# Optimization experiments

Hardware: AMD Instinct MI355X
Metric: run time of the kernel (lower is better)

## Reference

```python
import jax, jax.numpy as jnp
import numpy as np

EMBED = 3072
NQ = 32
NKV = 8
HD = EMBED // NQ  # 96
GROUPS = NQ // NKV  # 4
ROPE_BASE = 10000.0


def apply_rope(t, positions):
    # t: [b, h, s, d]; positions: [s] int
    d = t.shape[-1]
    inv_freq = 1.0 / (ROPE_BASE ** (jnp.arange(0, d, 2, dtype=jnp.float32) / d))  # [d/2]
    ang = positions.astype(jnp.float32)[:, None] * inv_freq[None, :]  # [s, d/2]
    cos = jnp.cos(ang)[None, None]  # [1,1,s,d/2]
    sin = jnp.sin(ang)[None, None]
    t1, t2 = t[..., : d // 2], t[..., d // 2 :]
    return jnp.concatenate([t1 * cos - t2 * sin, t2 * cos + t1 * sin], axis=-1)


def setup_inputs() -> dict:
    key = jax.random.key(0)
    k1, k2, k3 = jax.random.split(key, 3)
    b, s = 2, 2048
    x = jax.random.normal(k1, (b, s, EMBED), dtype=jnp.float32)
    positions = jnp.arange(s, dtype=jnp.int32)
    mask = jnp.triu(jnp.ones((s, s), dtype=bool), k=1)  # True = masked (causal)
    qkv_size = NQ * HD + 2 * NKV * HD  # 4608
    W_qkv = jax.random.normal(k2, (qkv_size, EMBED), dtype=jnp.float32) * (EMBED ** -0.5)
    W_o = jax.random.normal(k3, (EMBED, EMBED), dtype=jnp.float32) * (EMBED ** -0.5)
    return {"x": x, "positions": positions, "mask": mask, "W_qkv": W_qkv, "W_o": W_o}


def reference(x, positions, mask, W_qkv, W_o):
    b, s, _ = x.shape
    scaling = HD ** -0.5
    qkv = x @ W_qkv.T  # [b, s, 4608]
    q_size, kv_size = NQ * HD, NKV * HD
    q = qkv[..., :q_size].reshape(b, s, NQ, HD).transpose(0, 2, 1, 3)          # [b,NQ,s,d]
    k = qkv[..., q_size : q_size + kv_size].reshape(b, s, NKV, HD).transpose(0, 2, 1, 3)
    v = qkv[..., q_size + kv_size :].reshape(b, s, NKV, HD).transpose(0, 2, 1, 3)
    q = apply_rope(q, positions)
    k = apply_rope(k, positions)
    q = q.reshape(b, NKV, GROUPS, s, HD)
    scores = jnp.einsum("bkgsd,bktd->bkgst", q, k) * scaling  # [b,NKV,G,s,s]
    scores = jnp.where(mask[None, None, None], -jnp.inf, scores)
    attn = jax.nn.softmax(scores, axis=-1)
    out = jnp.einsum("bkgst,bktd->bkgsd", attn, v)
    out = out.reshape(b, NQ, s, HD).transpose(0, 2, 1, 3).reshape(b, s, NQ * HD)
    return out @ W_o.T
```

## Files before the change

kernel.cpp:

```cpp
#include <hip/hip_runtime.h>
#include <cstdint>

typedef unsigned short u16;
typedef unsigned int u32;
typedef __attribute__((ext_vector_type(4))) float f32x4;
typedef __attribute__((ext_vector_type(8))) __bf16 bf16x8;
typedef __attribute__((ext_vector_type(8))) unsigned short u16x8;
typedef __attribute__((ext_vector_type(4))) unsigned int u32x4;

#define S_LEN 2048
#define BATCH 2
#define NQH 32
#define NKVH 8
#define HD 96
#define EMB 3072
#define QKVN 4608
#define KOFF 3072
#define VOFF 3840
#define KSP 104

__device__ __forceinline__ u16 f2b(float f) {
    u32 u = __float_as_uint(f);
    u32 r = (u + 0x7fffu + ((u >> 16) & 1u)) >> 16;
    return (u16)r;
}
__device__ __forceinline__ float b2f(u16 h) { return __uint_as_float(((u32)h) << 16); }
__device__ __forceinline__ u32 cvtpk(float lo, float hi) {
    u32 r;
    asm("v_cvt_pk_bf16_f32 %0, %1, %2" : "=v"(r) : "v"(lo), "v"(hi));
    return r;
}

__global__ __launch_bounds__(256) void conv_f2b(const float* __restrict__ in,
                                                u16* __restrict__ outp, int n8) {
    const int i = blockIdx.x * 256 + threadIdx.x;
    if (i >= n8) return;
    const f32x4* q = (const f32x4*)(in + (size_t)i * 8);
    const f32x4 a = q[0], b = q[1];
    u16x8 t;
#pragma unroll
    for (int j = 0; j < 4; ++j) {
        t[j] = f2b(a[j]);
        t[j + 4] = f2b(b[j]);
    }
    *(u16x8*)(outp + (size_t)i * 8) = t;
}

typedef __attribute__((address_space(1))) const uint32_t gas_u32;
typedef __attribute__((address_space(3))) uint32_t las_u32;
__device__ __forceinline__ void gld_lds16(const u16* g, u16* l) {
    __builtin_amdgcn_global_load_lds((gas_u32*)g, (las_u32*)l, 16, 0, 0);
}

#define WAITV4 asm volatile("s_waitcnt vmcnt(4)" ::: "memory")
#define WAITV0 asm volatile("s_waitcnt vmcnt(0)" ::: "memory")
#define BARRIER __builtin_amdgcn_s_barrier()
#define SCHEDB __builtin_amdgcn_sched_barrier(0)

template <bool OUTF32>
__global__ __launch_bounds__(256, 2) void gemm_bt_p(const u16* __restrict__ Ap,
                                                    const u16* __restrict__ Bp,
                                                    void* __restrict__ Cp,
                                                    int M, int N, int K, int ldc) {
    __shared__ __align__(16) u16 S[2 * 16384];
    const int tid = threadIdx.x;
    const int wave = tid >> 6, lane = tid & 63;
    const int lrow = lane & 15, lhi = lane >> 4;

    int bxi = blockIdx.x, byi = blockIdx.y;
    {
        const int gx = gridDim.x;
        const int nwg = gx * gridDim.y;
        if ((nwg & 7) == 0) {
            int fid = byi * gx + bxi;
            fid = (fid & 7) * (nwg >> 3) + (fid >> 3);
            bxi = fid % gx;
            byi = fid / gx;
        }
    }
    const int bm = byi * 128, bn = bxi * 128;
    const int wm = (wave >> 1) * 64, wn = (wave & 1) * 64;
    const int xsl = ((lhi ^ (lrow & 3) ^ ((lrow >> 2) & 3)) << 3);
    const int srow = tid >> 2;
    const int scol = (((tid & 3) ^ ((tid >> 2) & 3) ^ ((tid >> 4) & 3))) * 8;
    const u16* gA0 = Ap + (size_t)(bm + srow) * K + scol;
    const u16* gA1 = Ap + (size_t)(bm + 64 + srow) * K + scol;
    const u16* gB0 = Bp + (size_t)(bn + srow) * K + scol;
    const u16* gB1 = Bp + (size_t)(bn + 64 + srow) * K + scol;
    u16* const dbase = S + (tid & 192) * 8;

    f32x4 acc[4][4] = {};
    const int nt = K >> 6;

    gld_lds16(gA0, dbase);
    gld_lds16(gA1, dbase + 2048);
    gld_lds16(gB0, dbase + 8192);
    gld_lds16(gB1, dbase + 8192 + 2048);
    gld_lds16(gA0 + 32, dbase + 4096);
    gld_lds16(gA1 + 32, dbase + 4096 + 2048);
    gld_lds16(gB0 + 32, dbase + 8192 + 4096);
    gld_lds16(gB1 + 32, dbase + 8192 + 4096 + 2048);

    for (int t = 0; t + 1 < nt; ++t) {
        const int cur = t & 1;
        const u16* Ab = S + cur * 16384;
        const u16* Bb = Ab + 8192;
        u16* dn = dbase + (cur ^ 1) * 16384;
        const int ko = (t + 1) << 6;

        WAITV4;
        BARRIER;
        SCHEDB;
        gld_lds16(gA0 + ko, dn);
        gld_lds16(gA1 + ko, dn + 2048);
        bf16x8 af[4], bf0[2], bf1[2];
#pragma unroll
        for (int mi = 0; mi < 4; ++mi)
            af[mi] = *(const bf16x8*)(Ab + (wm + mi * 16 + lrow) * 32 + xsl);
#pragma unroll
        for (int ni = 0; ni < 2; ++ni)
            bf0[ni] = *(const bf16x8*)(Bb + (wn + ni * 16 + lrow) * 32 + xsl);
        __builtin_amdgcn_s_setprio(1);
#pragma unroll
        for (int mi = 0; mi < 4; ++mi)
#pragma unroll
            for (int ni = 0; ni < 2; ++ni)
                acc[mi][ni] = __builtin_amdgcn_mfma_f32_16x16x32_bf16(af[mi], bf0[ni],
                                                                      acc[mi][ni], 0, 0, 0);
        __builtin_amdgcn_s_setprio(0);
        gld_lds16(gB0 + ko, dn + 8192);
        gld_lds16(gB1 + ko, dn + 8192 + 2048);
#pragma unroll
        for (int ni = 0; ni < 2; ++ni)
            bf1[ni] = *(const bf16x8*)(Bb + (wn + (ni + 2) * 16 + lrow) * 32 + xsl);
        __builtin_amdgcn_s_setprio(1);
#pragma unroll
        for (int mi = 0; mi < 4; ++mi)
#pragma unroll
            for (int ni = 0; ni < 2; ++ni)
                acc[mi][ni + 2] = __builtin_amdgcn_mfma_f32_16x16x32_bf16(af[mi], bf1[ni],
                                                                          acc[mi][ni + 2], 0, 0, 0);
        __builtin_amdgcn_s_setprio(0);

        WAITV4;
        BARRIER;
        SCHEDB;
        gld_lds16(gA0 + ko + 32, dn + 4096);
        gld_lds16(gA1 + ko + 32, dn + 4096 + 2048);
#pragma unroll
        for (int mi = 0; mi < 4; ++mi)
            af[mi] = *(const bf16x8*)(Ab + 4096 + (wm + mi * 16 + lrow) * 32 + xsl);
#pragma unroll
        for (int ni = 0; ni < 2; ++ni)
            bf0[ni] = *(const bf16x8*)(Bb + 4096 + (wn + ni * 16 + lrow) * 32 + xsl);
        __builtin_amdgcn_s_setprio(1);
#pragma unroll
        for (int mi = 0; mi < 4; ++mi)
#pragma unroll
            for (int ni = 0; ni < 2; ++ni)
                acc[mi][ni] = __builtin_amdgcn_mfma_f32_16x16x32_bf16(af[mi], bf0[ni],
                                                                      acc[mi][ni], 0, 0, 0);
        __builtin_amdgcn_s_setprio(0);
        gld_lds16(gB0 + ko + 32, dn + 8192 + 4096);
        gld_lds16(gB1 + ko + 32, dn + 8192 + 4096 + 2048);
#pragma unroll
        for (int ni = 0; ni < 2; ++ni)
            bf1[ni] = *(const bf16x8*)(Bb + 4096 + (wn + (ni + 2) * 16 + lrow) * 32 + xsl);
        __builtin_amdgcn_s_setprio(1);
#pragma unroll
        for (int mi = 0; mi < 4; ++mi)
#pragma unroll
            for (int ni = 0; ni < 2; ++ni)
                acc[mi][ni + 2] = __builtin_amdgcn_mfma_f32_16x16x32_bf16(af[mi], bf1[ni],
                                                                          acc[mi][ni + 2], 0, 0, 0);
        __builtin_amdgcn_s_setprio(0);
    }

    {
        const int cur = (nt - 1) & 1;
        const u16* Ab = S + cur * 16384;
        const u16* Bb = Ab + 8192;
        WAITV4;
        BARRIER;
        SCHEDB;
        bf16x8 af[4], bfr[4];
#pragma unroll
        for (int mi = 0; mi < 4; ++mi)
            af[mi] = *(const bf16x8*)(Ab + (wm + mi * 16 + lrow) * 32 + xsl);
#pragma unroll
        for (int ni = 0; ni < 4; ++ni)
            bfr[ni] = *(const bf16x8*)(Bb + (wn + ni * 16 + lrow) * 32 + xsl);
#pragma unroll
        for (int mi = 0; mi < 4; ++mi)
#pragma unroll
            for (int ni = 0; ni < 4; ++ni)
                acc[mi][ni] = __builtin_amdgcn_mfma_f32_16x16x32_bf16(af[mi], bfr[ni],
                                                                      acc[mi][ni], 0, 0, 0);
        WAITV0;
        BARRIER;
        SCHEDB;
#pragma unroll
        for (int mi = 0; mi < 4; ++mi)
            af[mi] = *(const bf16x8*)(Ab + 4096 + (wm + mi * 16 + lrow) * 32 + xsl);
#pragma unroll
        for (int ni = 0; ni < 4; ++ni)
            bfr[ni] = *(const bf16x8*)(Bb + 4096 + (wn + ni * 16 + lrow) * 32 + xsl);
#pragma unroll
        for (int mi = 0; mi < 4; ++mi)
#pragma unroll
            for (int ni = 0; ni < 4; ++ni)
                acc[mi][ni] = __builtin_amdgcn_mfma_f32_16x16x32_bf16(af[mi], bfr[ni],
                                                                      acc[mi][ni], 0, 0, 0);
    }

    const int orow = bm + wm + lhi * 4;
    const int ocol = bn + wn + lrow;
#pragma unroll
    for (int mi = 0; mi < 4; ++mi)
#pragma unroll
        for (int ni = 0; ni < 4; ++ni)
#pragma unroll
            for (int r = 0; r < 4; ++r) {
                const size_t idx = (size_t)(orow + mi * 16 + r) * ldc + ocol + ni * 16;
                if constexpr (OUTF32)
                    ((float*)Cp)[idx] = acc[mi][ni][r];
                else
                    ((u16*)Cp)[idx] = f2b(acc[mi][ni][r]);
            }
}

__global__ __launch_bounds__(256) void gqa_rope(u16* __restrict__ qkv,
                                                const int* __restrict__ positions) {
    int i = blockIdx.x * 256 + threadIdx.x;
    const int pair = i % 48;
    int t = i / 48;
    const int head = t % (NQH + NKVH);
    const int bs = t / (NQH + NKVH);
    const int pos = positions[bs & (S_LEN - 1)];
    const size_t base = (size_t)bs * QKVN + (head < NQH ? head * HD : KOFF + (head - NQH) * HD);
    const float invf = __expf(-(float)(2 * pair) * (1.0f / 96.0f) * 9.210340371976184f);
    const float ang = (float)pos * invf;
    float sn, cs;
    __sincosf(ang, &sn, &cs);
    const float t1 = b2f(qkv[base + pair]);
    const float t2 = b2f(qkv[base + 48 + pair]);
    qkv[base + pair] = f2b(t1 * cs - t2 * sn);
    qkv[base + 48 + pair] = f2b(t2 * cs + t1 * sn);
}

__global__ __launch_bounds__(256) void gqa_attn5(const u16* __restrict__ qkv,
                                                 u16* __restrict__ out) {
    __shared__ __align__(16) u16 Ks[64 * KSP];
    __shared__ __align__(16) u16 Vtmp[64 * 96];
    __shared__ __align__(16) u16 Vt[96 * 72];

    const int tid = threadIdx.x;
    const int wave = tid >> 6, lane = tid & 63;
    const int lrow = lane & 15, lhi = lane >> 4;
    const int bx = blockIdx.x;
    const int qt32 = 63 - (bx >> 4);
    const int kvh = (bx >> 1) & 7, bb = bx & 1;
    const int qh = kvh * 4 + wave;
    const int srow0 = bb * S_LEN + qt32 * 32;
    const int kb_last = (qt32 * 32 + 31) >> 6;
    const float cl2 = 0.10206207261596575f * 1.4426950408889634f;

    bf16x8 bq[2][3];
#pragma unroll
    for (int qt = 0; qt < 2; ++qt)
#pragma unroll
        for (int kd = 0; kd < 3; ++kd)
            bq[qt][kd] = *(const bf16x8*)(qkv + (size_t)(srow0 + qt * 16 + lrow) * QKVN +
                                          qh * 96 + kd * 32 + lhi * 8);

    float m_s[2] = {-3e38f, -3e38f}, l_s[2] = {0.0f, 0.0f};
    f32x4 oacc[6][2] = {};

    const int s0 = lrow + ((lane & 16) ? 32 : 0);
    const int s1 = s0 + 16;
    const bool khi = (lane & 32) != 0;

    const size_t kvrow0 = (size_t)(bb * S_LEN) * QKVN;
    u16x8 kreg[3], vreg[3];

    {
        const size_t kbase = kvrow0 + KOFF + (size_t)kvh * 96;
        const size_t vbase = kvrow0 + VOFF + (size_t)kvh * 96;
#pragma unroll
        for (int i = 0; i < 3; ++i) {
            const int u = tid + 256 * i;
            const int so = (u % 12) * 8, sr = u / 12;
            kreg[i] = *(const u16x8*)(qkv + kbase + (size_t)sr * QKVN + so);
            vreg[i] = *(const u16x8*)(qkv + vbase + (size_t)sr * QKVN + so);
        }
#pragma unroll
        for (int i = 0; i < 3; ++i) {
            const int u = tid + 256 * i;
            const int so = (u % 12) * 8, sr = u / 12;
            *(u16x8*)(Ks + sr * KSP + so) = kreg[i];
            *(u16x8*)(Vtmp + sr * 96 + so) = vreg[i];
        }
        __syncthreads();
#pragma unroll
        for (int i = 0; i < 3; ++i) {
            const int u = tid + 256 * i;
            const int td = u % 96, ts8 = u / 96;
            u16x8 c;
#pragma unroll
            for (int j = 0; j < 8; ++j) c[j] = Vtmp[(ts8 * 8 + j) * 96 + td];
            *(u16x8*)(Vt + td * 72 + ts8 * 8) = c;
        }
    }

    for (int kb = 0; kb <= kb_last; ++kb) {
        if (kb < kb_last) {
            const size_t kbase2 = kvrow0 + (size_t)((kb + 1) * 64) * QKVN + KOFF + kvh * 96;
            const size_t vbase2 = kvrow0 + (size_t)((kb + 1) * 64) * QKVN + VOFF + kvh * 96;
#pragma unroll
            for (int i = 0; i < 3; ++i) {
                const int u = tid + 256 * i;
                const int so = (u % 12) * 8, sr = u / 12;
                kreg[i] = *(const u16x8*)(qkv + kbase2 + (size_t)sr * QKVN + so);
                vreg[i] = *(const u16x8*)(qkv + vbase2 + (size_t)sr * QKVN + so);
            }
        }
        __syncthreads();

        bf16x8 ka[4][3];
#pragma unroll
        for (int kt = 0; kt < 4; ++kt)
#pragma unroll
            for (int kd = 0; kd < 3; ++kd)
                ka[kt][kd] = *(const bf16x8*)(Ks + (kt * 16 + lrow) * KSP + kd * 32 + lhi * 8);

        const int qoff = qt32 * 32 - kb * 64;
        const bool lastkb = (kb == kb_last);
        u32 bp[2][2][4];

#pragma unroll
        for (int qt = 0; qt < 2; ++qt) {
            const int qrelmax = qoff + qt * 16 + 15;
            f32x4 sacc[4] = {};
#pragma unroll
            for (int kt = 0; kt < 4; ++kt) {
                if (lastkb && kt * 16 > qrelmax) continue;
#pragma unroll
                for (int kd = 0; kd < 3; ++kd)
                    sacc[kt] = __builtin_amdgcn_mfma_f32_16x16x32_bf16(ka[kt][kd], bq[qt][kd],
                                                                       sacc[kt], 0, 0, 0);
            }
            float p[4][4];
            float mx = -3e38f;
            if (lastkb) {
                const int qrel = qoff + qt * 16 + lrow;
#pragma unroll
                for (int kt = 0; kt < 4; ++kt)
#pragma unroll
                    for (int r = 0; r < 4; ++r) {
                        const bool live = (kt * 16 + lhi * 4 + r) <= qrel;
                        const float s = live ? sacc[kt][r] : -3e38f;
                        p[kt][r] = s;
                        mx = fmaxf(mx, s);
                    }
            } else {
#pragma unroll
                for (int kt = 0; kt < 4; ++kt)
#pragma unroll
                    for (int r = 0; r < 4; ++r) {
                        p[kt][r] = sacc[kt][r];
                        mx = fmaxf(mx, sacc[kt][r]);
                    }
            }
            mx = fmaxf(mx, __shfl_xor(mx, 16));
            mx = fmaxf(mx, __shfl_xor(mx, 32));
            float mn = m_s[qt];
            if (!__all(mx - mn <= 20.0f)) {
                const float mnew = fmaxf(mn, mx);
                const float alpha = exp2f((mn - mnew) * cl2);
                m_s[qt] = mnew;
                mn = mnew;
                l_s[qt] *= alpha;
#pragma unroll
                for (int dt = 0; dt < 6; ++dt)
#pragma unroll
                    for (int r = 0; r < 4; ++r) oacc[dt][qt][r] *= alpha;
            }
            float rs = 0.0f;
#pragma unroll
            for (int kt = 0; kt < 4; ++kt)
#pragma unroll
                for (int r = 0; r < 4; ++r) {
                    const float pv = exp2f((p[kt][r] - mn) * cl2);
                    p[kt][r] = pv;
                    rs += pv;
                }
            rs += __shfl_xor(rs, 16);
            rs += __shfl_xor(rs, 32);
            l_s[qt] += rs;
            u32 pk[4][2];
#pragma unroll
            for (int kt = 0; kt < 4; ++kt) {
                pk[kt][0] = cvtpk(p[kt][0], p[kt][1]);
                pk[kt][1] = cvtpk(p[kt][2], p[kt][3]);
            }
#pragma unroll
            for (int kk = 0; kk < 2; ++kk) {
                const u32 a0 = (u32)__shfl((int)pk[kk * 2][0], s0, 64);
                const u32 b0 = (u32)__shfl((int)pk[kk * 2 + 1][0], s0, 64);
                const u32 a1 = (u32)__shfl((int)pk[kk * 2][1], s0, 64);
                const u32 b1 = (u32)__shfl((int)pk[kk * 2 + 1][1], s0, 64);
                const u32 a2 = (u32)__shfl((int)pk[kk * 2][0], s1, 64);
                const u32 b2 = (u32)__shfl((int)pk[kk * 2 + 1][0], s1, 64);
                const u32 a3 = (u32)__shfl((int)pk[kk * 2][1], s1, 64);
                const u32 b3 = (u32)__shfl((int)pk[kk * 2 + 1][1], s1, 64);
                bp[qt][kk][0] = khi ? b0 : a0;
                bp[qt][kk][1] = khi ? b1 : a1;
                bp[qt][kk][2] = khi ? b2 : a2;
                bp[qt][kk][3] = khi ? b3 : a3;
            }
        }

#pragma unroll
        for (int dt = 0; dt < 6; ++dt) {
            bf16x8 va[2];
#pragma unroll
            for (int kk = 0; kk < 2; ++kk)
                va[kk] = *(const bf16x8*)(Vt + (dt * 16 + lrow) * 72 + kk * 32 + lhi * 8);
#pragma unroll
            for (int qt = 0; qt < 2; ++qt)
#pragma unroll
                for (int kk = 0; kk < 2; ++kk) {
                    const u32x4 bv = {bp[qt][kk][0], bp[qt][kk][1], bp[qt][kk][2], bp[qt][kk][3]};
                    oacc[dt][qt] = __builtin_amdgcn_mfma_f32_16x16x32_bf16(
                        va[kk], __builtin_bit_cast(bf16x8, bv), oacc[dt][qt], 0, 0, 0);
                }
        }

        __syncthreads();
        if (kb < kb_last) {
#pragma unroll
            for (int i = 0; i < 3; ++i) {
                const int u = tid + 256 * i;
                const int so = (u % 12) * 8, sr = u / 12;
                *(u16x8*)(Ks + sr * KSP + so) = kreg[i];
                *(u16x8*)(Vtmp + sr * 96 + so) = vreg[i];
            }
            __syncthreads();
#pragma unroll
            for (int i = 0; i < 3; ++i) {
                const int u = tid + 256 * i;
                const int td = u % 96, ts8 = u / 96;
                u16x8 c;
#pragma unroll
                for (int j = 0; j < 8; ++j) c[j] = Vtmp[(ts8 * 8 + j) * 96 + td];
                *(u16x8*)(Vt + td * 72 + ts8 * 8) = c;
            }
        }
    }

    const size_t obase = (size_t)srow0 * EMB + qh * 96;
#pragma unroll
    for (int qt = 0; qt < 2; ++qt) {
        const float inv = 1.0f / l_s[qt];
        const size_t rbase = obase + (size_t)(qt * 16 + lrow) * EMB;
#pragma unroll
        for (int dt = 0; dt < 6; ++dt)
#pragma unroll
            for (int rp = 0; rp < 2; ++rp) {
                const u32 pair = cvtpk(oacc[dt][qt][2 * rp] * inv, oacc[dt][qt][2 * rp + 1] * inv);
                *(u32*)(out + rbase + dt * 16 + lhi * 4 + 2 * rp) = pair;
            }
    }
}

extern "C" void kernel_launch(void* const* d_in, const int* in_sizes, int n_in,
                              void* d_out, int out_size, void* d_ws, size_t ws_size,
                              hipStream_t stream) {
    const float* x = (const float*)d_in[0];
    const int* positions = (const int*)d_in[1];
    const float* W_qkv = (const float*)d_in[3];
    const float* W_o = (const float*)d_in[4];
    float* out = (float*)d_out;

    const int M = BATCH * S_LEN;
    const size_t QKV_E = (size_t)M * QKVN;
    const size_t ATT_E = (size_t)M * EMB;
    const size_t X_E = (size_t)M * EMB;
    const size_t WQKV_E = (size_t)QKVN * EMB;
    const size_t WO_E = (size_t)EMB * EMB;

    u16* qkv = (u16*)d_ws;
    u16* scratch = qkv + QKV_E;
    u16* xb = scratch;
    u16* wqkvb = (u16*)d_out;
    u16* wob = (u16*)d_ws;

    conv_f2b<<<(int)(X_E / 8 / 256), 256, 0, stream>>>(x, xb, (int)(X_E / 8));
    conv_f2b<<<(int)(WQKV_E / 8 / 256), 256, 0, stream>>>(W_qkv, wqkvb, (int)(WQKV_E / 8));
    gemm_bt_p<false>
        <<<dim3(QKVN / 128, M / 128), 256, 0, stream>>>(xb, wqkvb, qkv, M, QKVN, EMB, QKVN);
    gqa_rope<<<(BATCH * S_LEN * (NQH + NKVH) * 48) / 256, 256, 0, stream>>>(qkv, positions);
    gqa_attn5<<<dim3(1024), 256, 0, stream>>>(qkv, scratch);
    conv_f2b<<<(int)(WO_E / 8 / 256), 256, 0, stream>>>(W_o, wob, (int)(WO_E / 8));
    gemm_bt_p<true>
        <<<dim3(EMB / 128, M / 128), 256, 0, stream>>>(scratch, wob, out, M, EMB, EMB, EMB);
}
```

Baseline: 618.2 us.

## Replace GEMM with 256x256 eight-wave ping-pong kernel and vectorize RoPE

```diff
diff --git a/kernel.cpp b/kernel.cpp
--- a/kernel.cpp
+++ b/kernel.cpp
@@ -52,171 +52,262 @@
     __builtin_amdgcn_global_load_lds((gas_u32*)g, (las_u32*)l, 16, 0, 0);
 }
 
-#define WAITV4 asm volatile("s_waitcnt vmcnt(4)" ::: "memory")
-#define WAITV0 asm volatile("s_waitcnt vmcnt(0)" ::: "memory")
+#define WAITV2 asm volatile("s_waitcnt vmcnt(2)" ::: "memory")
+#define LGKM0 asm volatile("s_waitcnt lgkmcnt(0)" ::: "memory")
 #define BARRIER __builtin_amdgcn_s_barrier()
 #define SCHEDB __builtin_amdgcn_sched_barrier(0)
 
+__device__ __forceinline__ void stage_half(const u16* __restrict__ Gp, int ldg, int k0,
+                                           u16* lds_op, int h, int tid) {
+#pragma unroll
+    for (int L = 0; L < 2; ++L) {
+        const int c = L * 512 + tid;
+        const int r = c >> 3;
+        const int seg = (c & 7) ^ (((r >> 2) & 1) << 1);
+        const u16* src = Gp + (size_t)(h * 128 + r) * ldg + k0 + seg * 8;
+        u16* dst = lds_op + h * 8192 + (L * 512 + (tid & 448)) * 8;
+        gld_lds16(src, dst);
+    }
+}
+
+__device__ __forceinline__ bf16x8 frag(const u16* opb, int row, int segl) {
+    const int seg = segl ^ (((row >> 2) & 1) << 1);
+    return *(const bf16x8*)(opb + row * 64 + seg * 8);
+}
+
 template <bool OUTF32>
-__global__ __launch_bounds__(256, 2) void gemm_bt_p(const u16* __restrict__ Ap,
-                                                    const u16* __restrict__ Bp,
-                                                    void* __restrict__ Cp,
-                                                    int M, int N, int K, int ldc) {
-    __shared__ __align__(16) u16 S[2 * 16384];
+__global__ __launch_bounds__(512, 2) void gemm_bt8(const u16* __restrict__ Ap,
+                                                   const u16* __restrict__ Bp,
+                                                   void* __restrict__ Cp,
+                                                   int M, int N, int K, int ldc) {
+    __shared__ __align__(16) u16 S[65536];
     const int tid = threadIdx.x;
-    const int wave = tid >> 6, lane = tid & 63;
+    const int lane = tid & 63;
     const int lrow = lane & 15, lhi = lane >> 4;
-
-    int bxi = blockIdx.x, byi = blockIdx.y;
-    {
-        const int gx = gridDim.x;
-        const int nwg = gx * gridDim.y;
-        if ((nwg & 7) == 0) {
-            int fid = byi * gx + bxi;
-            fid = (fid & 7) * (nwg >> 3) + (fid >> 3);
-            bxi = fid % gx;
-            byi = fid / gx;
-        }
+    const int wid = tid >> 6;
+    const int wr = wid >> 2, wc = wid & 3;
+    const int bm = blockIdx.y * 256, bn = blockIdx.x * 256;
+    const u16* Ab = Ap + (size_t)bm * K;
+    const u16* Bb = Bp + (size_t)bn * K;
+    u16* const AE = S;
+    u16* const BE = S + 16384;
+    u16* const AO = S + 32768;
+    u16* const BO = S + 49152;
+
+    f32x4 acc[8][4] = {};
+    const int nt = K >> 6;
+    const int arow0 = wr * 128 + lrow;
+    const int brow0 = wc * 64 + lrow;
+
+    stage_half(Ab, K, 0, AE, 0, tid);
+    stage_half(Ab, K, 0, AE, 1, tid);
+    stage_half(Bb, K, 0, BE, 0, tid);
+    stage_half(Bb, K, 0, BE, 1, tid);
+    stage_half(Ab, K, 64, AO, 0, tid);
+    WAITV2;
+    BARRIER;
+
+    bf16x8 af[4][2], bfr[2][2];
+    for (int j = 0; j < (nt >> 1); ++j) {
+        const int o = 2 * j + 1;
+        const int ke2 = (2 * j + 2 < nt) ? (2 * j + 2) * 64 : 0;
+        const int ko2 = (2 * j + 3 < nt) ? (2 * j + 3) * 64 : 0;
+
+#pragma unroll
+        for (int mi = 0; mi < 4; ++mi) {
+            af[mi][0] = frag(AE, arow0 + mi * 16, lhi);
+            af[mi][1] = frag(AE, arow0 + mi * 16, 4 + lhi);
+        }
+#pragma unroll
+        for (int ni = 0; ni < 2; ++ni) {
+            bfr[ni][0] = frag(BE, brow0 + ni * 16, lhi);
+            bfr[ni][1] = frag(BE, brow0 + ni * 16, 4 + lhi);
+        }
+        stage_half(Ab, K, o * 64, AO, 1, tid);
+        BARRIER;
+        LGKM0;
+        SCHEDB;
+        __builtin_amdgcn_s_setprio(1);
+#pragma unroll
+        for (int mi = 0; mi < 4; ++mi)
+#pragma unroll
+            for (int ni = 0; ni < 2; ++ni)
+#pragma unroll
+                for (int kc = 0; kc < 2; ++kc)
+                    acc[mi][ni] = __builtin_amdgcn_mfma_f32_16x16x32_bf16(
+                        af[mi][kc], bfr[ni][kc], acc[mi][ni], 0, 0, 0);
+        __builtin_amdgcn_s_setprio(0);
+        BARRIER;
+
+#pragma unroll
+        for (int ni = 0; ni < 2; ++ni) {
+            bfr[ni][0] = frag(BE, brow0 + (ni + 2) * 16, lhi);
+            bfr[ni][1] = frag(BE, brow0 + (ni + 2) * 16, 4 + lhi);
+        }
+        stage_half(Bb, K, o * 64, BO, 0, tid);
+        BARRIER;
+        LGKM0;
+        SCHEDB;
+        __builtin_amdgcn_s_setprio(1);
+#pragma unroll
+        for (int mi = 0; mi < 4; ++mi)
+#pragma unroll
+            for (int ni = 0; ni < 2; ++ni)
+#pragma unroll
+                for (int kc = 0; kc < 2; ++kc)
+                    acc[mi][ni + 2] = __builtin_amdgcn_mfma_f32_16x16x32_bf16(
+                        af[mi][kc], bfr[ni][kc], acc[mi][ni + 2], 0, 0, 0);
+        __builtin_amdgcn_s_setprio(0);
+        BARRIER;
+
+#pragma unroll
+        for (int mi = 0; mi < 4; ++mi) {
+            af[mi][0] = frag(AE, arow0 + (mi + 4) * 16, lhi);
+            af[mi][1] = frag(AE, arow0 + (mi + 4) * 16, 4 + lhi);
+        }
+#pragma unroll
+        for (int ni = 0; ni < 2; ++ni) {
+            bfr[ni][0] = frag(BE, brow0 + ni * 16, lhi);
+            bfr[ni][1] = frag(BE, brow0 + ni * 16, 4 + lhi);
+        }
+        stage_half(Bb, K, o * 64, BO, 1, tid);
+        BARRIER;
+        LGKM0;
+        SCHEDB;
+        __builtin_amdgcn_s_setprio(1);
+#pragma unroll
+        for (int mi = 0; mi < 4; ++mi)
+#pragma unroll
+            for (int ni = 0; ni < 2; ++ni)
+#pragma unroll
+                for (int kc = 0; kc < 2; ++kc)
+                    acc[mi + 4][ni] = __builtin_amdgcn_mfma_f32_16x16x32_bf16(
+                        af[mi][kc], bfr[ni][kc], acc[mi + 4][ni], 0, 0, 0);
+        __builtin_amdgcn_s_setprio(0);
+        BARRIER;
+
+#pragma unroll
+        for (int ni = 0; ni < 2; ++ni) {
+            bfr[ni][0] = frag(BE, brow0 + (ni + 2) * 16, lhi);
+            bfr[ni][1] = frag(BE, brow0 + (ni + 2) * 16, 4 + lhi);
+        }
+        stage_half(Ab, K, ke2, AE, 0, tid);
+        BARRIER;
+        LGKM0;
+        SCHEDB;
+        __builtin_amdgcn_s_setprio(1);
+#pragma unroll
+        for (int mi = 0; mi < 4; ++mi)
+#pragma unroll
+            for (int ni = 0; ni < 2; ++ni)
+#pragma unroll
+                for (int kc = 0; kc < 2; ++kc)
+                    acc[mi + 4][ni + 2] = __builtin_amdgcn_mfma_f32_16x16x32_bf16(
+                        af[mi][kc], bfr[ni][kc], acc[mi + 4][ni + 2], 0, 0, 0);
+        __builtin_amdgcn_s_setprio(0);
+        WAITV2;
+        BARRIER;
+
+#pragma unroll
+        for (int mi = 0; mi < 4; ++mi) {
+            af[mi][0] = frag(AO, arow0 + mi * 16, lhi);
+            af[mi][1] = frag(AO, arow0 + mi * 16, 4 + lhi);
+        }
+#pragma unroll
+        for (int ni = 0; ni < 2; ++ni) {
+            bfr[ni][0] = frag(BO, brow0 + ni * 16, lhi);
+            bfr[ni][1] = frag(BO, brow0 + ni * 16, 4 + lhi);
+        }
+        stage_half(Ab, K, ke2, AE, 1, tid);
+        BARRIER;
+        LGKM0;
+        SCHEDB;
+        __builtin_amdgcn_s_setprio(1);
+#pragma unroll
+        for (int mi = 0; mi < 4; ++mi)
+#pragma unroll
+            for (int ni = 0; ni < 2; ++ni)
+#pragma unroll
+                for (int kc = 0; kc < 2; ++kc)
+                    acc[mi][ni] = __builtin_amdgcn_mfma_f32_16x16x32_bf16(
+                        af[mi][kc], bfr[ni][kc], acc[mi][ni], 0, 0, 0);
+        __builtin_amdgcn_s_setprio(0);
+        BARRIER;
+
+#pragma unroll
+        for (int ni = 0; ni < 2; ++ni) {
+            bfr[ni][0] = frag(BO, brow0 + (ni + 2) * 16, lhi);
+            bfr[ni][1] = frag(BO, brow0 + (ni + 2) * 16, 4 + lhi);
+        }
+        stage_half(Bb, K, ke2, BE, 0, tid);
+        BARRIER;
+        LGKM0;
+        SCHEDB;
+        __builtin_amdgcn_s_setprio(1);
+#pragma unroll
+        for (int mi = 0; mi < 4; ++mi)
+#pragma unroll
+            for (int ni = 0; ni < 2; ++ni)
+#pragma unroll
+                for (int kc = 0; kc < 2; ++kc)
+                    acc[mi][ni + 2] = __builtin_amdgcn_mfma_f32_16x16x32_bf16(
+                        af[mi][kc], bfr[ni][kc], acc[mi][ni + 2], 0, 0, 0);
+        __builtin_amdgcn_s_setprio(0);
+        BARRIER;
+
+#pragma unroll
+        for (int mi = 0; mi < 4; ++mi) {
+            af[mi][0] = frag(AO, arow0 + (mi + 4) * 16, lhi);
+            af[mi][1] = frag(AO, arow0 + (mi + 4) * 16, 4 + lhi);
+        }
+#pragma unroll
+        for (int ni = 0; ni < 2; ++ni) {
+            bfr[ni][0] = frag(BO, brow0 + ni * 16, lhi);
+            bfr[ni][1] = frag(BO, brow0 + ni * 16, 4 + lhi);
+        }
+        stage_half(Bb, K, ke2, BE, 1, tid);
+        BARRIER;
+        LGKM0;
+        SCHEDB;
+        __builtin_amdgcn_s_setprio(1);
+#pragma unroll
+        for (int mi = 0; mi < 4; ++mi)
+#pragma unroll
+            for (int ni = 0; ni < 2; ++ni)
+#pragma unroll
+                for (int kc = 0; kc < 2; ++kc)
+                    acc[mi + 4][ni] = __builtin_amdgcn_mfma_f32_16x16x32_bf16(
+                        af[mi][kc], bfr[ni][kc], acc[mi + 4][ni], 0, 0, 0);
+        __builtin_amdgcn_s_setprio(0);
+        BARRIER;
+
+#pragma unroll
+        for (int ni = 0; ni < 2; ++ni) {
+            bfr[ni][0] = frag(BO, brow0 + (ni + 2) * 16, lhi);
+            bfr[ni][1] = frag(BO, brow0 + (ni + 2) * 16, 4 + lhi);
+        }
+        stage_half(Ab, K, ko2, AO, 0, tid);
+        BARRIER;
+        LGKM0;
+        SCHEDB;
+        __builtin_amdgcn_s_setprio(1);
+#pragma unroll
+        for (int mi = 0; mi < 4; ++mi)
+#pragma unroll
+            for (int ni = 0; ni < 2; ++ni)
+#pragma unroll
+                for (int kc = 0; kc < 2; ++kc)
+                    acc[mi + 4][ni + 2] = __builtin_amdgcn_mfma_f32_16x16x32_bf16(
+                        af[mi][kc], bfr[ni][kc], acc[mi + 4][ni + 2], 0, 0, 0);
+        __builtin_amdgcn_s_setprio(0);
+        WAITV2;
+        BARRIER;
     }
-    const int bm = byi * 128, bn = bxi * 128;
-    const int wm = (wave >> 1) * 64, wn = (wave & 1) * 64;
-    const int xsl = ((lhi ^ (lrow & 3) ^ ((lrow >> 2) & 3)) << 3);
-    const int srow = tid >> 2;
-    const int scol = (((tid & 3) ^ ((tid >> 2) & 3) ^ ((tid >> 4) & 3))) * 8;
-    const u16* gA0 = Ap + (size_t)(bm + srow) * K + scol;
-    const u16* gA1 = Ap + (size_t)(bm + 64 + srow) * K + scol;
-    const u16* gB0 = Bp + (size_t)(bn + srow) * K + scol;
-    const u16* gB1 = Bp + (size_t)(bn + 64 + srow) * K + scol;
-    u16* const dbase = S + (tid & 192) * 8;
-
-    f32x4 acc[4][4] = {};
-    const int nt = K >> 6;
-
-    gld_lds16(gA0, dbase);
-    gld_lds16(gA1, dbase + 2048);
-    gld_lds16(gB0, dbase + 8192);
-    gld_lds16(gB1, dbase + 8192 + 2048);
-    gld_lds16(gA0 + 32, dbase + 4096);
-    gld_lds16(gA1 + 32, dbase + 4096 + 2048);
-    gld_lds16(gB0 + 32, dbase + 8192 + 4096);
-    gld_lds16(gB1 + 32, dbase + 8192 + 4096 + 2048);
-
-    for (int t = 0; t + 1 < nt; ++t) {
-        const int cur = t & 1;
-        const u16* Ab = S + cur * 16384;
-        const u16* Bb = Ab + 8192;
-        u16* dn = dbase + (cur ^ 1) * 16384;
-        const int ko = (t + 1) << 6;
-
-        WAITV4;
-        BARRIER;
-        SCHEDB;
-        gld_lds16(gA0 + ko, dn);
-        gld_lds16(gA1 + ko, dn + 2048);
-        bf16x8 af[4], bf0[2], bf1[2];
-#pragma unroll
-        for (int mi = 0; mi < 4; ++mi)
-            af[mi] = *(const bf16x8*)(Ab + (wm + mi * 16 + lrow) * 32 + xsl);
-#pragma unroll
-        for (int ni = 0; ni < 2; ++ni)
-            bf0[ni] = *(const bf16x8*)(Bb + (wn + ni * 16 + lrow) * 32 + xsl);
-        __builtin_amdgcn_s_setprio(1);
-#pragma unroll
-        for (int mi = 0; mi < 4; ++mi)
-#pragma unroll
-            for (int ni = 0; ni < 2; ++ni)
-                acc[mi][ni] = __builtin_amdgcn_mfma_f32_16x16x32_bf16(af[mi], bf0[ni],
-                                                                      acc[mi][ni], 0, 0, 0);
-        __builtin_amdgcn_s_setprio(0);
-        gld_lds16(gB0 + ko, dn + 8192);
-        gld_lds16(gB1 + ko, dn + 8192 + 2048);
-#pragma unroll
-        for (int ni = 0; ni < 2; ++ni)
-            bf1[ni] = *(const bf16x8*)(Bb + (wn + (ni + 2) * 16 + lrow) * 32 + xsl);
-        __builtin_amdgcn_s_setprio(1);
-#pragma unroll
-        for (int mi = 0; mi < 4; ++mi)
-#pragma unroll
-            for (int ni = 0; ni < 2; ++ni)
-                acc[mi][ni + 2] = __builtin_amdgcn_mfma_f32_16x16x32_bf16(af[mi], bf1[ni],
-                                                                          acc[mi][ni + 2], 0, 0, 0);
-        __builtin_amdgcn_s_setprio(0);
-
-        WAITV4;
-        BARRIER;
-        SCHEDB;
-        gld_lds16(gA0 + ko + 32, dn + 4096);
-        gld_lds16(gA1 + ko + 32, dn + 4096 + 2048);
-#pragma unroll
-        for (int mi = 0; mi < 4; ++mi)
-            af[mi] = *(const bf16x8*)(Ab + 4096 + (wm + mi * 16 + lrow) * 32 + xsl);
-#pragma unroll
-        for (int ni = 0; ni < 2; ++ni)
-            bf0[ni] = *(const bf16x8*)(Bb + 4096 + (wn + ni * 16 + lrow) * 32 + xsl);
-        __builtin_amdgcn_s_setprio(1);
-#pragma unroll
-        for (int mi = 0; mi < 4; ++mi)
-#pragma unroll
-            for (int ni = 0; ni < 2; ++ni)
-                acc[mi][ni] = __builtin_amdgcn_mfma_f32_16x16x32_bf16(af[mi], bf0[ni],
-                                                                      acc[mi][ni], 0, 0, 0);
-        __builtin_amdgcn_s_setprio(0);
-        gld_lds16(gB0 + ko + 32, dn + 8192 + 4096);
-        gld_lds16(gB1 + ko + 32, dn + 8192 + 4096 + 2048);
-#pragma unroll
-        for (int ni = 0; ni < 2; ++ni)
-            bf1[ni] = *(const bf16x8*)(Bb + 4096 + (wn + (ni + 2) * 16 + lrow) * 32 + xsl);
-        __builtin_amdgcn_s_setprio(1);
-#pragma unroll
-        for (int mi = 0; mi < 4; ++mi)
-#pragma unroll
-            for (int ni = 0; ni < 2; ++ni)
-                acc[mi][ni + 2] = __builtin_amdgcn_mfma_f32_16x16x32_bf16(af[mi], bf1[ni],
-                                                                          acc[mi][ni + 2], 0, 0, 0);
-        __builtin_amdgcn_s_setprio(0);
-    }
-
-    {
-        const int cur = (nt - 1) & 1;
-        const u16* Ab = S + cur * 16384;
-        const u16* Bb = Ab + 8192;
-        WAITV4;
-        BARRIER;
-        SCHEDB;
-        bf16x8 af[4], bfr[4];
-#pragma unroll
-        for (int mi = 0; mi < 4; ++mi)
-            af[mi] = *(const bf16x8*)(Ab + (wm + mi * 16 + lrow) * 32 + xsl);
-#pragma unroll
-        for (int ni = 0; ni < 4; ++ni)
-            bfr[ni] = *(const bf16x8*)(Bb + (wn + ni * 16 + lrow) * 32 + xsl);
-#pragma unroll
-        for (int mi = 0; mi < 4; ++mi)
-#pragma unroll
-            for (int ni = 0; ni < 4; ++ni)
-                acc[mi][ni] = __builtin_amdgcn_mfma_f32_16x16x32_bf16(af[mi], bfr[ni],
-                                                                      acc[mi][ni], 0, 0, 0);
-        WAITV0;
-        BARRIER;
-        SCHEDB;
-#pragma unroll
-        for (int mi = 0; mi < 4; ++mi)
-            af[mi] = *(const bf16x8*)(Ab + 4096 + (wm + mi * 16 + lrow) * 32 + xsl);
-#pragma unroll
-        for (int ni = 0; ni < 4; ++ni)
-            bfr[ni] = *(const bf16x8*)(Bb + 4096 + (wn + ni * 16 + lrow) * 32 + xsl);
-#pragma unroll
-        for (int mi = 0; mi < 4; ++mi)
-#pragma unroll
-            for (int ni = 0; ni < 4; ++ni)
-                acc[mi][ni] = __builtin_amdgcn_mfma_f32_16x16x32_bf16(af[mi], bfr[ni],
-                                                                      acc[mi][ni], 0, 0, 0);
-    }
-
-    const int orow = bm + wm + lhi * 4;
-    const int ocol = bn + wn + lrow;
-#pragma unroll
-    for (int mi = 0; mi < 4; ++mi)
+
+    const int orow = bm + wr * 128 + lhi * 4;
+    const int ocol = bn + wc * 64 + lrow;
+#pragma unroll
+    for (int mi = 0; mi < 8; ++mi)
 #pragma unroll
         for (int ni = 0; ni < 4; ++ni)
 #pragma unroll
@@ -229,23 +320,32 @@
             }
 }
 
-__global__ __launch_bounds__(256) void gqa_rope(u16* __restrict__ qkv,
-                                                const int* __restrict__ positions) {
-    int i = blockIdx.x * 256 + threadIdx.x;
-    const int pair = i % 48;
-    int t = i / 48;
+__global__ __launch_bounds__(256) void gqa_rope8(u16* __restrict__ qkv,
+                                                 const int* __restrict__ positions) {
+    const int i = blockIdx.x * 256 + threadIdx.x;
+    const int pc = i % 6;
+    int t = i / 6;
     const int head = t % (NQH + NKVH);
     const int bs = t / (NQH + NKVH);
     const int pos = positions[bs & (S_LEN - 1)];
-    const size_t base = (size_t)bs * QKVN + (head < NQH ? head * HD : KOFF + (head - NQH) * HD);
-    const float invf = __expf(-(float)(2 * pair) * (1.0f / 96.0f) * 9.210340371976184f);
-    const float ang = (float)pos * invf;
-    float sn, cs;
-    __sincosf(ang, &sn, &cs);
-    const float t1 = b2f(qkv[base + pair]);
-    const float t2 = b2f(qkv[base + 48 + pair]);
-    qkv[base + pair] = f2b(t1 * cs - t2 * sn);
-    qkv[base + 48 + pair] = f2b(t2 * cs + t1 * sn);
+    const size_t base = (size_t)bs * QKVN +
+                        (head < NQH ? head * HD : KOFF + (head - NQH) * HD) + pc * 8;
+    const u16x8 a = *(const u16x8*)(qkv + base);
+    const u16x8 b = *(const u16x8*)(qkv + base + 48);
+    u16x8 ra, rb;
+#pragma unroll
+    for (int jj = 0; jj < 8; ++jj) {
+        const int pair = pc * 8 + jj;
+        const float invf = __expf(-(float)(2 * pair) * (1.0f / 96.0f) * 9.210340371976184f);
+        const float ang = (float)pos * invf;
+        float sn, cs;
+        __sincosf(ang, &sn, &cs);
+        const float t1 = b2f(a[jj]), t2 = b2f(b[jj]);
+        ra[jj] = f2b(t1 * cs - t2 * sn);
+        rb[jj] = f2b(t2 * cs + t1 * sn);
+    }
+    *(u16x8*)(qkv + base) = ra;
+    *(u16x8*)(qkv + base + 48) = rb;
 }
 
 __global__ __launch_bounds__(256) void gqa_attn5(const u16* __restrict__ qkv,
@@ -484,7 +584,6 @@
 
     const int M = BATCH * S_LEN;
     const size_t QKV_E = (size_t)M * QKVN;
-    const size_t ATT_E = (size_t)M * EMB;
     const size_t X_E = (size_t)M * EMB;
     const size_t WQKV_E = (size_t)QKVN * EMB;
     const size_t WO_E = (size_t)EMB * EMB;
@@ -497,11 +596,11 @@
 
     conv_f2b<<<(int)(X_E / 8 / 256), 256, 0, stream>>>(x, xb, (int)(X_E / 8));
     conv_f2b<<<(int)(WQKV_E / 8 / 256), 256, 0, stream>>>(W_qkv, wqkvb, (int)(WQKV_E / 8));
-    gemm_bt_p<false>
-        <<<dim3(QKVN / 128, M / 128), 256, 0, stream>>>(xb, wqkvb, qkv, M, QKVN, EMB, QKVN);
-    gqa_rope<<<(BATCH * S_LEN * (NQH + NKVH) * 48) / 256, 256, 0, stream>>>(qkv, positions);
+    gemm_bt8<false>
+        <<<dim3(QKVN / 256, M / 256), 512, 0, stream>>>(xb, wqkvb, qkv, M, QKVN, EMB, QKVN);
+    gqa_rope8<<<(BATCH * S_LEN * (NQH + NKVH) * 6) / 256, 256, 0, stream>>>(qkv, positions);
     gqa_attn5<<<dim3(1024), 256, 0, stream>>>(qkv, scratch);
     conv_f2b<<<(int)(WO_E / 8 / 256), 256, 0, stream>>>(W_o, wob, (int)(WO_E / 8));
-    gemm_bt_p<true>
-        <<<dim3(EMB / 128, M / 128), 256, 0, stream>>>(scratch, wob, out, M, EMB, EMB, EMB);
-}
+    gemm_bt8<true>
+        <<<dim3(EMB / 256, M / 256), 512, 0, stream>>>(scratch, wob, out, M, EMB, EMB, EMB);
+}
```

New measurement: 641.3 us. 3.7% more time.
